# Kernel tuning notes

Hardware: AMD Instinct MI355X
Metric: run time of the kernel (lower is better)

Reference implementation:

```python
import math
import jax, jax.numpy as jnp
import numpy as np

B, N, D, H = 2, 8192, 1024, 16


def setup_inputs() -> dict:
    key = jax.random.key(0)
    k1, k2, k3, k4 = jax.random.split(key, 4)
    s = 1.0 / math.sqrt(D)
    return {
        "x": jax.random.normal(k1, (B, N, D), dtype=jnp.float32),
        "W_qk": jax.random.normal(k2, (D, D), dtype=jnp.float32) * s,
        "W_v": jax.random.normal(k3, (D, D), dtype=jnp.float32) * s,
        "W_out": jax.random.normal(k4, (D, D), dtype=jnp.float32) * s,
        "tau": jnp.ones((H, 1, 1), dtype=jnp.float32),
    }


def reference(x, W_qk, W_v, W_out, tau):
    b, n, d = x.shape
    h = H
    dh = d // h
    # QK / V projections (no bias), then to channel-major (B, H, dh, N)
    qk = (x @ W_qk).transpose(0, 2, 1).reshape(b, h, dh, n)
    v = (x @ W_v).transpose(0, 2, 1).reshape(b, h, dh, n)
    # Cross-channel Gram matrix over tokens: (B, H, dh, dh)
    dot = jnp.einsum('bhcn,bhdn->bhcd', qk, qk)
    q2 = jnp.sum(qk * qk, axis=-1)  # (B, H, dh)
    # Negative squared Euclidean distance between channel vectors
    logits = (2.0 * dot - q2[:, :, :, None] - q2[:, :, None, :]) / math.sqrt(max(n, 1))
    logits = logits * tau[None, ...]
    attn = jax.nn.softmax(logits, axis=-1)  # (B, H, dh, dh)
    w = jnp.einsum('bhcd,bhdn->bhcn', attn, v)  # (B, H, dh, N)
    out = w.reshape(b, d, n).transpose(0, 2, 1) @ W_out  # (B, N, D)
    return out
```

## Files before the change

kernel.cpp:

```cpp
#include <hip/hip_runtime.h>
#include <hip/hip_bf16.h>
#include <cstdint>
#include <cstddef>

typedef __bf16 v8bf __attribute__((ext_vector_type(8)));
typedef float  v4f  __attribute__((ext_vector_type(4)));

__device__ __forceinline__ unsigned short f2bf(float f) {
    unsigned int u = __float_as_uint(f);
    u += 0x7fffu + ((u >> 16) & 1u);
    return (unsigned short)(u >> 16);
}

__device__ __forceinline__ void gload_lds16(const unsigned short* g, unsigned short* l) {
    __builtin_amdgcn_global_load_lds(
        (const __attribute__((address_space(1))) unsigned int*)(uintptr_t)g,
        (__attribute__((address_space(3))) unsigned int*)(uintptr_t)l, 16, 0, 0);
}

template<int WRITE_BF16>
__global__ __launch_bounds__(256, 2) void gemm_bt(
    const unsigned short* __restrict__ A,
    const unsigned short* __restrict__ BT,
    void* __restrict__ C,
    int K, int lda, int ldb, int ldc,
    size_t sAz, size_t sBz, size_t sCz)
{
    __shared__ unsigned short sA[128 * 32];
    __shared__ unsigned short sB[128 * 32];

    const unsigned short* Ab = A + (size_t)blockIdx.z * sAz;
    const unsigned short* Bb = BT + (size_t)blockIdx.z * sBz;

    const int tid  = threadIdx.x;
    const int wv   = tid >> 6;
    const int lane = tid & 63;
    const int quad = lane >> 4;
    const int l16  = lane & 15;
    const size_t bm = (size_t)blockIdx.y * 128;
    const size_t bn = (size_t)blockIdx.x * 128;
    const int wm = (wv >> 1) * 64;
    const int wn = (wv & 1) * 64;

    const int ro = tid >> 2;
    const int ko = (((tid & 3) ^ (ro & 3)) << 3);

    const unsigned short* aptr0 = Ab + (bm + ro)      * (size_t)lda + ko;
    const unsigned short* aptr1 = Ab + (bm + ro + 64) * (size_t)lda + ko;
    const unsigned short* bptr0 = Bb + (bn + ro)      * (size_t)ldb + ko;
    const unsigned short* bptr1 = Bb + (bn + ro + 64) * (size_t)ldb + ko;

    unsigned short* sA0 = &sA[wv * 512];
    unsigned short* sA1 = &sA[2048 + wv * 512];
    unsigned short* sB0 = &sB[wv * 512];
    unsigned short* sB1 = &sB[2048 + wv * 512];

    const int sslot = ((quad ^ (l16 & 3)) << 3);

    v4f acc[4][4] = {};

    for (int k0 = 0; k0 < K; k0 += 32) {
        gload_lds16(aptr0 + k0, sA0);
        gload_lds16(aptr1 + k0, sA1);
        gload_lds16(bptr0 + k0, sB0);
        gload_lds16(bptr1 + k0, sB1);
        __syncthreads();

        v8bf af[4], bfr[4];
        #pragma unroll
        for (int t = 0; t < 4; t++) {
            af[t]  = *(const v8bf*)&sA[(size_t)(wm + t * 16 + l16) * 32 + sslot];
            bfr[t] = *(const v8bf*)&sB[(size_t)(wn + t * 16 + l16) * 32 + sslot];
        }

        #pragma unroll
        for (int ti = 0; ti < 4; ti++)
            #pragma unroll
            for (int tj = 0; tj < 4; tj++)
                acc[ti][tj] = __builtin_amdgcn_mfma_f32_16x16x32_bf16(
                    af[ti], bfr[tj], acc[ti][tj], 0, 0, 0);
        __syncthreads();
    }

    if (WRITE_BF16) {
        unsigned short* Cb = (unsigned short*)C + (size_t)blockIdx.z * sCz;
        #pragma unroll
        for (int ti = 0; ti < 4; ti++) {
            const size_t row0 = bm + wm + ti * 16 + quad * 4;
            #pragma unroll
            for (int tj = 0; tj < 4; tj++) {
                const size_t col = bn + wn + tj * 16 + l16;
                #pragma unroll
                for (int r = 0; r < 4; r++)
                    Cb[(row0 + r) * (size_t)ldc + col] = f2bf(acc[ti][tj][r]);
            }
        }
    } else {
        float* Cb = (float*)C + (size_t)blockIdx.z * sCz;
        #pragma unroll
        for (int ti = 0; ti < 4; ti++) {
            const size_t row0 = bm + wm + ti * 16 + quad * 4;
            #pragma unroll
            for (int tj = 0; tj < 4; tj++) {
                const size_t col = bn + wn + tj * 16 + l16;
                #pragma unroll
                for (int r = 0; r < 4; r++)
                    Cb[(row0 + r) * (size_t)ldc + col] = acc[ti][tj][r];
            }
        }
    }
}

__global__ __launch_bounds__(256) void gram_kernel(
    const unsigned short* __restrict__ qk,
    float* __restrict__ partial)
{
    const int bh = blockIdx.x;
    const int split = blockIdx.y;
    const int b = bh >> 4, h = bh & 15;
    const unsigned short* base = qk + (size_t)b * 8192 * 1024 + (size_t)h * 64;
    const int n0 = split * 1024;

    __shared__ unsigned short sMT[64 * 136];
    const int tid = threadIdx.x;
    const int wv = tid >> 6, lane = tid & 63, quad = lane >> 4, l16 = lane & 15;

    v4f acc[4] = {};

    for (int chunk = 0; chunk < 8; chunk++) {
        const int nb = n0 + chunk * 128;
        __syncthreads();
        #pragma unroll
        for (int i = 0; i < 4; i++) {
            const int ch = tid + i * 256;
            const int tok = ch >> 3;
            const int co = (ch & 7) << 3;
            union { uint4 v; unsigned short s[8]; } u;
            u.v = *(const uint4*)(base + (size_t)(nb + tok) * 1024 + co);
            #pragma unroll
            for (int j = 0; j < 8; j++)
                sMT[(size_t)(co + j) * 136 + tok] = u.s[j];
        }
        __syncthreads();

        #pragma unroll
        for (int ks = 0; ks < 4; ks++) {
            const int kb = ks * 32 + quad * 8;
            const v8bf a = *(const v8bf*)&sMT[(size_t)(16 * wv + l16) * 136 + kb];
            #pragma unroll
            for (int t = 0; t < 4; t++) {
                const v8bf bb = *(const v8bf*)&sMT[(size_t)(t * 16 + l16) * 136 + kb];
                acc[t] = __builtin_amdgcn_mfma_f32_16x16x32_bf16(a, bb, acc[t], 0, 0, 0);
            }
        }
    }

    float* outp = partial + ((size_t)split * 32 + bh) * 4096;
    #pragma unroll
    for (int t = 0; t < 4; t++)
        #pragma unroll
        for (int r = 0; r < 4; r++)
            outp[(size_t)(16 * wv + quad * 4 + r) * 64 + t * 16 + l16] = acc[t][r];
}

__global__ __launch_bounds__(256) void softmax_kernel(
    const float* __restrict__ partial,
    const float* __restrict__ tau,
    float* __restrict__ attn)
{
    const int gw = (int)((blockIdx.x * 256 + threadIdx.x) >> 6);
    const int d = threadIdx.x & 63;
    const int bh = gw >> 6;
    const int c = gw & 63;
    const int h = bh & 15;

    float cd = 0.f, cc = 0.f, dd = 0.f;
    #pragma unroll
    for (int s = 0; s < 8; s++) {
        const float* p = partial + ((size_t)s * 32 + bh) * 4096;
        cd += p[c * 64 + d];
        cc += p[c * 65];
        dd += p[d * 65];
    }
    const float INV_SQRT_N = 0.011048543456039806f;
    const float logit = (2.f * cd - cc - dd) * INV_SQRT_N * tau[h];

    float m = logit;
    #pragma unroll
    for (int off = 32; off > 0; off >>= 1) m = fmaxf(m, __shfl_xor(m, off, 64));
    const float e = __expf(logit - m);
    float sum = e;
    #pragma unroll
    for (int off = 32; off > 0; off >>= 1) sum += __shfl_xor(sum, off, 64);

    attn[(size_t)bh * 4096 + c * 64 + d] = e / sum;
}

__global__ __launch_bounds__(256) void wefft_kernel(
    const float* __restrict__ attn,
    const float* __restrict__ Wout,
    unsigned short* __restrict__ weffT)
{
    const int bh = blockIdx.x;
    const int jg = blockIdx.y;
    const int b = bh >> 4, h = bh & 15;

    __shared__ float sAttT[64][65];
    __shared__ float sW[64][65];
    const int tid = threadIdx.x;
    const float* ap = attn + (size_t)bh * 4096;
    const float* wp = Wout + (size_t)(h * 64) * 1024 + jg * 64;
    for (int i = tid; i < 4096; i += 256) {
        const int cc = i >> 6, q = i & 63;
        sAttT[q][cc] = ap[i];
        sW[cc][q] = wp[(size_t)cc * 1024 + q];
    }
    __syncthreads();

    const int dd0 = (tid >> 4) << 2;
    const int j0  = (tid & 15) << 2;
    float acc[4][4] = {};
    for (int cc = 0; cc < 64; cc++) {
        float av[4], wvv[4];
        #pragma unroll
        for (int i = 0; i < 4; i++) av[i] = sAttT[dd0 + i][cc];
        #pragma unroll
        for (int i = 0; i < 4; i++) wvv[i] = sW[cc][j0 + i];
        #pragma unroll
        for (int i = 0; i < 4; i++)
            #pragma unroll
            for (int j = 0; j < 4; j++)
                acc[i][j] += av[i] * wvv[j];
    }

    unsigned short* op = weffT + ((size_t)b * 1024 + jg * 64) * 1024 + h * 64;
    #pragma unroll
    for (int i = 0; i < 4; i++)
        #pragma unroll
        for (int j = 0; j < 4; j++)
            op[(size_t)(j0 + j) * 1024 + dd0 + i] = f2bf(acc[i][j]);
}

__global__ __launch_bounds__(256) void cvt_x_kernel(
    const float* __restrict__ x, unsigned short* __restrict__ xb)
{
    const size_t i = ((size_t)blockIdx.x * 256 + threadIdx.x) * 4;
    const float4 v = *(const float4*)(x + i);
    ushort4 o;
    o.x = f2bf(v.x); o.y = f2bf(v.y); o.z = f2bf(v.z); o.w = f2bf(v.w);
    *(ushort4*)(xb + i) = o;
}

__global__ void cvt_wT_kernel(const float* __restrict__ W,
                              unsigned short* __restrict__ WT)
{
    __shared__ float s[32][33];
    const int n0 = blockIdx.x * 32;
    const int k0 = blockIdx.y * 32;
    for (int i = threadIdx.y; i < 32; i += 8)
        s[i][threadIdx.x] = W[(size_t)(k0 + i) * 1024 + n0 + threadIdx.x];
    __syncthreads();
    for (int i = threadIdx.y; i < 32; i += 8)
        WT[(size_t)(n0 + i) * 1024 + k0 + threadIdx.x] = f2bf(s[threadIdx.x][i]);
}

extern "C" void kernel_launch(void* const* d_in, const int* in_sizes, int n_in,
                              void* d_out, int out_size, void* d_ws, size_t ws_size,
                              hipStream_t stream)
{
    (void)in_sizes; (void)n_in; (void)out_size; (void)ws_size;
    const float* x    = (const float*)d_in[0];
    const float* Wqk  = (const float*)d_in[1];
    const float* Wv   = (const float*)d_in[2];
    const float* Wout = (const float*)d_in[3];
    const float* tau  = (const float*)d_in[4];

    unsigned short* xb     = (unsigned short*)d_ws;
    unsigned short* wqkT   = xb + (size_t)16384 * 1024;
    unsigned short* wvb    = wqkT + (size_t)1024 * 1024;
    unsigned short* qk     = wvb + (size_t)1024 * 1024;
    float*          partial= (float*)(qk + (size_t)16384 * 1024);
    float*          attn   = partial + (size_t)8 * 32 * 4096;
    unsigned short* weffT  = (unsigned short*)(attn + (size_t)32 * 4096);
    unsigned short* wfoldT = weffT + (size_t)2 * 1024 * 1024;

    cvt_x_kernel<<<16384, 256, 0, stream>>>(x, xb);
    cvt_x_kernel<<<1024, 256, 0, stream>>>(Wv, wvb);
    cvt_wT_kernel<<<dim3(32, 32), dim3(32, 8), 0, stream>>>(Wqk, wqkT);

    gemm_bt<1><<<dim3(8, 128, 1), 256, 0, stream>>>(
        xb, wqkT, (void*)qk, 1024, 1024, 1024, 1024, 0, 0, 0);

    gram_kernel<<<dim3(32, 8), 256, 0, stream>>>(qk, partial);
    softmax_kernel<<<512, 256, 0, stream>>>(partial, tau, attn);
    wefft_kernel<<<dim3(32, 16), 256, 0, stream>>>(attn, Wout, weffT);

    gemm_bt<1><<<dim3(8, 8, 2), 256, 0, stream>>>(
        weffT, wvb, (void*)wfoldT, 1024, 1024, 1024, 1024,
        (size_t)1024 * 1024, 0, (size_t)1024 * 1024);

    gemm_bt<0><<<dim3(8, 64, 2), 256, 0, stream>>>(
        xb, wfoldT, d_out, 1024, 1024, 1024, 1024,
        (size_t)8192 * 1024, (size_t)1024 * 1024, (size_t)8192 * 1024);
}
```

Baseline: 280.9 us.

## Add XCD-aware GEMM tile mapping, split gram wider with prefetch, fuse conversion kernels

The GEMM grid becomes 1D, and each XCD (blockIdx mod 8) gets a contiguous band of M tiles so L2 reuse of the A and B tiles improves. The gram kernel now uses 16 token splits instead of 8 and register-prefetches the next chunk, which doubles the partial buffer the softmax reduces. The softmax writes attention transposed so wefft loads it coalesced. The three conversion kernels are merged into one launch to cut launch overhead.

```diff
diff --git a/kernel.cpp b/kernel.cpp
--- a/kernel.cpp
+++ b/kernel.cpp
@@ -24,21 +24,31 @@
     const unsigned short* __restrict__ BT,
     void* __restrict__ C,
     int K, int lda, int ldb, int ldc,
-    size_t sAz, size_t sBz, size_t sCz)
+    size_t sAz, size_t sBz, size_t sCz,
+    int nBlk, int mPerXcd)
 {
     __shared__ unsigned short sA[128 * 32];
     __shared__ unsigned short sB[128 * 32];
 
-    const unsigned short* Ab = A + (size_t)blockIdx.z * sAz;
-    const unsigned short* Bb = BT + (size_t)blockIdx.z * sBz;
+    const int id = blockIdx.x;
+    const int xcd = id & 7;
+    int s = id >> 3;
+    const int perXcd = mPerXcd * nBlk;
+    const int z = s / perXcd;
+    s -= z * perXcd;
+    const int mB = xcd * mPerXcd + s / nBlk;
+    const int nB = s - (s / nBlk) * nBlk;
+
+    const unsigned short* Ab = A + (size_t)z * sAz;
+    const unsigned short* Bb = BT + (size_t)z * sBz;
 
     const int tid  = threadIdx.x;
     const int wv   = tid >> 6;
     const int lane = tid & 63;
     const int quad = lane >> 4;
     const int l16  = lane & 15;
-    const size_t bm = (size_t)blockIdx.y * 128;
-    const size_t bn = (size_t)blockIdx.x * 128;
+    const size_t bm = (size_t)mB * 128;
+    const size_t bn = (size_t)nB * 128;
     const int wm = (wv >> 1) * 64;
     const int wn = (wv & 1) * 64;
 
@@ -83,7 +93,7 @@
     }
 
     if (WRITE_BF16) {
-        unsigned short* Cb = (unsigned short*)C + (size_t)blockIdx.z * sCz;
+        unsigned short* Cb = (unsigned short*)C + (size_t)z * sCz;
         #pragma unroll
         for (int ti = 0; ti < 4; ti++) {
             const size_t row0 = bm + wm + ti * 16 + quad * 4;
@@ -96,7 +106,7 @@
             }
         }
     } else {
-        float* Cb = (float*)C + (size_t)blockIdx.z * sCz;
+        float* Cb = (float*)C + (size_t)z * sCz;
         #pragma unroll
         for (int ti = 0; ti < 4; ti++) {
             const size_t row0 = bm + wm + ti * 16 + quad * 4;
@@ -119,29 +129,41 @@
     const int split = blockIdx.y;
     const int b = bh >> 4, h = bh & 15;
     const unsigned short* base = qk + (size_t)b * 8192 * 1024 + (size_t)h * 64;
-    const int n0 = split * 1024;
+    const int n0 = split * 512;
 
     __shared__ unsigned short sMT[64 * 136];
     const int tid = threadIdx.x;
     const int wv = tid >> 6, lane = tid & 63, quad = lane >> 4, l16 = lane & 15;
 
+    uint4 pre[4];
+    #pragma unroll
+    for (int i = 0; i < 4; i++) {
+        const int ch = tid + i * 256, tok = ch >> 3, co = (ch & 7) << 3;
+        pre[i] = *(const uint4*)(base + (size_t)(n0 + tok) * 1024 + co);
+    }
+
     v4f acc[4] = {};
 
-    for (int chunk = 0; chunk < 8; chunk++) {
-        const int nb = n0 + chunk * 128;
+    for (int chunk = 0; chunk < 4; chunk++) {
         __syncthreads();
         #pragma unroll
         for (int i = 0; i < 4; i++) {
-            const int ch = tid + i * 256;
-            const int tok = ch >> 3;
-            const int co = (ch & 7) << 3;
-            union { uint4 v; unsigned short s[8]; } u;
-            u.v = *(const uint4*)(base + (size_t)(nb + tok) * 1024 + co);
+            const int ch = tid + i * 256, tok = ch >> 3, co = (ch & 7) << 3;
+            union { uint4 v; unsigned short s8[8]; } u; u.v = pre[i];
             #pragma unroll
             for (int j = 0; j < 8; j++)
-                sMT[(size_t)(co + j) * 136 + tok] = u.s[j];
-        }
-        __syncthreads();
+                sMT[(size_t)(co + j) * 136 + tok] = u.s8[j];
+        }
+        __syncthreads();
+
+        if (chunk < 3) {
+            const int nb = n0 + (chunk + 1) * 128;
+            #pragma unroll
+            for (int i = 0; i < 4; i++) {
+                const int ch = tid + i * 256, tok = ch >> 3, co = (ch & 7) << 3;
+                pre[i] = *(const uint4*)(base + (size_t)(nb + tok) * 1024 + co);
+            }
+        }
 
         #pragma unroll
         for (int ks = 0; ks < 4; ks++) {
@@ -166,7 +188,7 @@
 __global__ __launch_bounds__(256) void softmax_kernel(
     const float* __restrict__ partial,
     const float* __restrict__ tau,
-    float* __restrict__ attn)
+    float* __restrict__ attnT)
 {
     const int gw = (int)((blockIdx.x * 256 + threadIdx.x) >> 6);
     const int d = threadIdx.x & 63;
@@ -176,7 +198,7 @@
 
     float cd = 0.f, cc = 0.f, dd = 0.f;
     #pragma unroll
-    for (int s = 0; s < 8; s++) {
+    for (int s = 0; s < 16; s++) {
         const float* p = partial + ((size_t)s * 32 + bh) * 4096;
         cd += p[c * 64 + d];
         cc += p[c * 65];
@@ -193,11 +215,11 @@
     #pragma unroll
     for (int off = 32; off > 0; off >>= 1) sum += __shfl_xor(sum, off, 64);
 
-    attn[(size_t)bh * 4096 + c * 64 + d] = e / sum;
+    attnT[(size_t)bh * 4096 + d * 64 + c] = e / sum;
 }
 
 __global__ __launch_bounds__(256) void wefft_kernel(
-    const float* __restrict__ attn,
+    const float* __restrict__ attnT,
     const float* __restrict__ Wout,
     unsigned short* __restrict__ weffT)
 {
@@ -208,12 +230,12 @@
     __shared__ float sAttT[64][65];
     __shared__ float sW[64][65];
     const int tid = threadIdx.x;
-    const float* ap = attn + (size_t)bh * 4096;
+    const float* ap = attnT + (size_t)bh * 4096;
     const float* wp = Wout + (size_t)(h * 64) * 1024 + jg * 64;
     for (int i = tid; i < 4096; i += 256) {
-        const int cc = i >> 6, q = i & 63;
-        sAttT[q][cc] = ap[i];
-        sW[cc][q] = wp[(size_t)cc * 1024 + q];
+        const int r = i >> 6, q = i & 63;
+        sAttT[r][q] = ap[i];
+        sW[r][q] = wp[(size_t)r * 1024 + q];
     }
     __syncthreads();
 
@@ -241,27 +263,35 @@
             op[(size_t)(j0 + j) * 1024 + dd0 + i] = f2bf(acc[i][j]);
 }
 
-__global__ __launch_bounds__(256) void cvt_x_kernel(
-    const float* __restrict__ x, unsigned short* __restrict__ xb)
-{
-    const size_t i = ((size_t)blockIdx.x * 256 + threadIdx.x) * 4;
-    const float4 v = *(const float4*)(x + i);
-    ushort4 o;
-    o.x = f2bf(v.x); o.y = f2bf(v.y); o.z = f2bf(v.z); o.w = f2bf(v.w);
-    *(ushort4*)(xb + i) = o;
-}
-
-__global__ void cvt_wT_kernel(const float* __restrict__ W,
-                              unsigned short* __restrict__ WT)
-{
-    __shared__ float s[32][33];
-    const int n0 = blockIdx.x * 32;
-    const int k0 = blockIdx.y * 32;
-    for (int i = threadIdx.y; i < 32; i += 8)
-        s[i][threadIdx.x] = W[(size_t)(k0 + i) * 1024 + n0 + threadIdx.x];
-    __syncthreads();
-    for (int i = threadIdx.y; i < 32; i += 8)
-        WT[(size_t)(n0 + i) * 1024 + k0 + threadIdx.x] = f2bf(s[threadIdx.x][i]);
+__global__ __launch_bounds__(256) void cvt_all_kernel(
+    const float* __restrict__ x, const float* __restrict__ Wv,
+    const float* __restrict__ Wqk,
+    unsigned short* __restrict__ xb, unsigned short* __restrict__ wvb,
+    unsigned short* __restrict__ wqkT)
+{
+    const int bid = blockIdx.x;
+    if (bid < 17408) {
+        const float* src = (bid < 16384) ? x : Wv;
+        unsigned short* dst = (bid < 16384) ? xb : wvb;
+        const size_t blk = (bid < 16384) ? bid : (bid - 16384);
+        const size_t i = (blk * 256 + threadIdx.x) * 4;
+        const float4 v = *(const float4*)(src + i);
+        ushort4 o;
+        o.x = f2bf(v.x); o.y = f2bf(v.y); o.z = f2bf(v.z); o.w = f2bf(v.w);
+        *(ushort4*)(dst + i) = o;
+    } else {
+        const int t = bid - 17408;
+        const int n0 = (t & 31) * 32, k0 = (t >> 5) * 32;
+        __shared__ float sT[32][33];
+        const int tx = threadIdx.x & 31, ty = threadIdx.x >> 5;
+        #pragma unroll
+        for (int i = ty; i < 32; i += 8)
+            sT[i][tx] = Wqk[(size_t)(k0 + i) * 1024 + n0 + tx];
+        __syncthreads();
+        #pragma unroll
+        for (int i = ty; i < 32; i += 8)
+            wqkT[(size_t)(n0 + i) * 1024 + k0 + tx] = f2bf(sT[tx][i]);
+    }
 }
 
 extern "C" void kernel_launch(void* const* d_in, const int* in_sizes, int n_in,
@@ -280,26 +310,24 @@
     unsigned short* wvb    = wqkT + (size_t)1024 * 1024;
     unsigned short* qk     = wvb + (size_t)1024 * 1024;
     float*          partial= (float*)(qk + (size_t)16384 * 1024);
-    float*          attn   = partial + (size_t)8 * 32 * 4096;
-    unsigned short* weffT  = (unsigned short*)(attn + (size_t)32 * 4096);
+    float*          attnT  = partial + (size_t)16 * 32 * 4096;
+    unsigned short* weffT  = (unsigned short*)(attnT + (size_t)32 * 4096);
     unsigned short* wfoldT = weffT + (size_t)2 * 1024 * 1024;
 
-    cvt_x_kernel<<<16384, 256, 0, stream>>>(x, xb);
-    cvt_x_kernel<<<1024, 256, 0, stream>>>(Wv, wvb);
-    cvt_wT_kernel<<<dim3(32, 32), dim3(32, 8), 0, stream>>>(Wqk, wqkT);
-
-    gemm_bt<1><<<dim3(8, 128, 1), 256, 0, stream>>>(
-        xb, wqkT, (void*)qk, 1024, 1024, 1024, 1024, 0, 0, 0);
-
-    gram_kernel<<<dim3(32, 8), 256, 0, stream>>>(qk, partial);
-    softmax_kernel<<<512, 256, 0, stream>>>(partial, tau, attn);
-    wefft_kernel<<<dim3(32, 16), 256, 0, stream>>>(attn, Wout, weffT);
-
-    gemm_bt<1><<<dim3(8, 8, 2), 256, 0, stream>>>(
+    cvt_all_kernel<<<18432, 256, 0, stream>>>(x, Wv, Wqk, xb, wvb, wqkT);
+
+    gemm_bt<1><<<1024, 256, 0, stream>>>(
+        xb, wqkT, (void*)qk, 1024, 1024, 1024, 1024, 0, 0, 0, 8, 16);
+
+    gram_kernel<<<dim3(32, 16), 256, 0, stream>>>(qk, partial);
+    softmax_kernel<<<512, 256, 0, stream>>>(partial, tau, attnT);
+    wefft_kernel<<<dim3(32, 16), 256, 0, stream>>>(attnT, Wout, weffT);
+
+    gemm_bt<1><<<128, 256, 0, stream>>>(
         weffT, wvb, (void*)wfoldT, 1024, 1024, 1024, 1024,
-        (size_t)1024 * 1024, 0, (size_t)1024 * 1024);
-
-    gemm_bt<0><<<dim3(8, 64, 2), 256, 0, stream>>>(
+        (size_t)1024 * 1024, 0, (size_t)1024 * 1024, 8, 1);
+
+    gemm_bt<0><<<1024, 256, 0, stream>>>(
         xb, wfoldT, d_out, 1024, 1024, 1024, 1024,
-        (size_t)8192 * 1024, (size_t)1024 * 1024, (size_t)8192 * 1024);
-}
+        (size_t)8192 * 1024, (size_t)1024 * 1024, (size_t)8192 * 1024, 8, 8);
+}
```

After: 266.5 us. 5.1% less time.
